# Optimization experiments

Measured on AMD Instinct MI355X. Metric: run time of the kernel, lower is better.

## Reference

```python
import jax, jax.numpy as jnp
import numpy as np

C = 512
GROUPS = 32
EPS = 1e-6

def setup_inputs() -> dict:
    key = jax.random.key(0)
    ks = jax.random.split(key, 6)
    s = 1.0 / np.sqrt(C)
    return {
        "x": jax.random.normal(ks[0], (2, C, 16, 32, 32), dtype=jnp.float32),
        "gamma": jnp.ones((C,), jnp.float32),
        "beta": jnp.zeros((C,), jnp.float32),
        "q_w": jax.random.normal(ks[1], (C, C), jnp.float32) * s,
        "q_b": jnp.zeros((C,), jnp.float32),
        "k_w": jax.random.normal(ks[2], (C, C), jnp.float32) * s,
        "k_b": jnp.zeros((C,), jnp.float32),
        "v_w": jax.random.normal(ks[3], (C, C), jnp.float32) * s,
        "v_b": jnp.zeros((C,), jnp.float32),
        "proj_w": jax.random.normal(ks[4], (C, C), jnp.float32) * s,
        "proj_b": jnp.zeros((C,), jnp.float32),
    }

def _group_norm(x, gamma, beta):
    # x: [b, c, t, h, w]
    b, c, t, h, w = x.shape
    xg = x.reshape(b, GROUPS, c // GROUPS, t, h, w)
    mean = xg.mean(axis=(2, 3, 4, 5), keepdims=True)
    var = xg.var(axis=(2, 3, 4, 5), keepdims=True)
    xg = (xg - mean) * jax.lax.rsqrt(var + EPS)
    x = xg.reshape(b, c, t, h, w)
    return x * gamma[None, :, None, None, None] + beta[None, :, None, None, None]

def _pw_conv(x, w, bias):
    # 1x1x1 conv == channel GEMM. x: [b,c,t,h,w], w: [c_out, c_in]
    y = jnp.einsum('bcthw,oc->bothw', x, w)
    return y + bias[None, :, None, None, None]

def reference(x, gamma, beta, q_w, q_b, k_w, k_b, v_w, v_b, proj_w, proj_b):
    b, c, t, h, w = x.shape
    hn = _group_norm(x, gamma, beta)
    q = _pw_conv(hn, q_w, q_b)
    k = _pw_conv(hn, k_w, k_b)
    v = _pw_conv(hn, v_w, v_b)
    # [b,c,t,h,w] -> [b*t, h*w, c]
    def to_seq(a):
        return jnp.transpose(a, (0, 2, 3, 4, 1)).reshape(b * t, h * w, c)
    q, k, v = to_seq(q), to_seq(k), to_seq(v)
    scale = 1.0 / jnp.sqrt(jnp.asarray(c, x.dtype))
    attn = jnp.einsum('bqc,bkc->bqk', q, k) * scale  # [b*t, hw, hw]
    attn = jax.nn.softmax(attn, axis=-1)
    out = jnp.einsum('bqk,bkc->bqc', attn, v)
    out = out.reshape(b, t, h, w, c).transpose(0, 4, 1, 2, 3)
    return x + _pw_conv(out, proj_w, proj_b)
```

## Files before the change

### kernel.cpp

```cpp
#include <hip/hip_runtime.h>

typedef unsigned short u16;
typedef __attribute__((ext_vector_type(8))) short bf16x8;
typedef __attribute__((ext_vector_type(4))) float f32x4;

#define DEV static __device__ __forceinline__

DEV u16 f2bf(float f) {
  union { float f; unsigned u; } x; x.f = f;
  return (u16)((x.u + 0x7FFFu + ((x.u >> 16) & 1u)) >> 16);
}
DEV float bf2f(u16 h) { union { unsigned u; float f; } x; x.u = ((unsigned)h) << 16; return x.f; }

DEV void gload16(const void* g, void* l) {
  __builtin_amdgcn_global_load_lds((const __attribute__((address_space(1))) void*)g,
                                   (__attribute__((address_space(3))) void*)l, 16, 0, 0);
}

__global__ __launch_bounds__(256) void gn_stats_a(const float* __restrict__ x,
                                                  float2* __restrict__ part) {
  const int bg = blockIdx.x >> 5, slice = blockIdx.x & 31;
  const float* base = x + (long)bg * 262144 + slice * 8192;
  float s = 0.f, q = 0.f;
#pragma unroll
  for (int i = 0; i < 8; ++i) {
    float4 v = *(const float4*)(base + i * 1024 + threadIdx.x * 4);
    s += v.x + v.y + v.z + v.w;
    q += v.x * v.x + v.y * v.y + v.z * v.z + v.w * v.w;
  }
#pragma unroll
  for (int o = 32; o; o >>= 1) { s += __shfl_xor(s, o); q += __shfl_xor(q, o); }
  __shared__ float2 red[4];
  if ((threadIdx.x & 63) == 0) red[threadIdx.x >> 6] = make_float2(s, q);
  __syncthreads();
  if (threadIdx.x == 0) {
    float S = 0.f, Q = 0.f;
    for (int i = 0; i < 4; ++i) { S += red[i].x; Q += red[i].y; }
    part[blockIdx.x] = make_float2(S, Q);
  }
}

__global__ void gn_stats_b(const float2* __restrict__ part, float2* __restrict__ stats) {
  float s = 0.f, q = 0.f;
  if (threadIdx.x < 32) {
    float2 p = part[blockIdx.x * 32 + threadIdx.x];
    s = p.x; q = p.y;
  }
#pragma unroll
  for (int o = 32; o; o >>= 1) { s += __shfl_xor(s, o); q += __shfl_xor(q, o); }
  if (threadIdx.x == 0) {
    const float inv = 1.f / 262144.f;
    float mean = s * inv;
    float var = q * inv - mean * mean;
    stats[blockIdx.x] = make_float2(mean, rsqrtf(var + 1e-6f));
  }
}

__global__ __launch_bounds__(256) void gn_apply(const float* __restrict__ x,
                                                const float* __restrict__ gamma,
                                                const float* __restrict__ beta,
                                                const float2* __restrict__ stats,
                                                u16* __restrict__ hn) {
  __shared__ u16 tile[64][65];
  const int p0 = blockIdx.x * 64, c0 = blockIdx.y * 64, bt = blockIdx.z;
  const int b = bt >> 4, t = bt & 15, tid = threadIdx.x;
  const float* xb = x + (long)b * 8388608 + t * 1024;
#pragma unroll 4
  for (int r = 0; r < 16; ++r) {
    int ci = r * 4 + (tid >> 6), pi = tid & 63;
    int c = c0 + ci;
    float2 st = stats[b * 32 + (c >> 4)];
    float v = xb[(long)c * 16384 + p0 + pi];
    v = (v - st.x) * st.y * gamma[c] + beta[c];
    tile[ci][pi] = f2bf(v);
  }
  __syncthreads();
  u16* hb = hn + ((long)bt * 1024 + p0) * 512 + c0;
#pragma unroll 4
  for (int r = 0; r < 16; ++r) {
    int pi = r * 4 + (tid >> 6), ci = tid & 63;
    hb[(long)pi * 512 + ci] = tile[ci][pi];
  }
}

__global__ __launch_bounds__(256) void wconv(const float* __restrict__ w0, const float* __restrict__ w1,
                                             const float* __restrict__ w2, const float* __restrict__ w3,
                                             u16* __restrict__ dst) {
  int e = (blockIdx.x * 256 + threadIdx.x) * 4;
  const float* src = w0;
  int which = e >> 18, off = e & 262143;
  if (which == 1) src = w1; else if (which == 2) src = w2; else if (which == 3) src = w3;
  float4 v = *(const float4*)(src + off);
  ushort4 o;
  o.x = f2bf(v.x); o.y = f2bf(v.y); o.z = f2bf(v.z); o.w = f2bf(v.w);
  *(ushort4*)(dst + e) = o;
}

__global__ void bcat(const float* __restrict__ qb, const float* __restrict__ kb,
                     const float* __restrict__ vb, float* __restrict__ dst) {
  int i = blockIdx.x * 256 + threadIdx.x;
  if (i < 512) dst[i] = qb[i];
  else if (i < 1024) dst[i] = kb[i - 512];
  else if (i < 1536) dst[i] = vb[i - 1024];
}

__global__ __launch_bounds__(256) void transpose_pc(const u16* __restrict__ v, int ldv,
                                                    u16* __restrict__ vT) {
  __shared__ u16 tile[64][65];
  const int p0 = blockIdx.x * 64, c0 = blockIdx.y * 64;
  const long bt = blockIdx.z;
  const int tid = threadIdx.x;
  const u16* vb = v + bt * 1024 * (long)ldv;
#pragma unroll 4
  for (int r = 0; r < 16; ++r) {
    int pi = r * 4 + (tid >> 6), ci = tid & 63;
    tile[pi][ci] = vb[(long)(p0 + pi) * ldv + c0 + ci];
  }
  __syncthreads();
  u16* ob = vT + bt * 524288;
#pragma unroll 4
  for (int r = 0; r < 16; ++r) {
    int ci = r * 4 + (tid >> 6), pi = tid & 63;
    ob[(long)(c0 + ci) * 1024 + p0 + pi] = tile[pi][ci];
  }
}

__global__ __launch_bounds__(256) void softmax_rows_bf16(u16* __restrict__ scores) {
  const int wave = threadIdx.x >> 6, lane = threadIdx.x & 63;
  const long row = (long)blockIdx.x * 4 + wave;
  u16* srow = scores + row * 1024;
  bf16x8 a0 = *(const bf16x8*)(srow + lane * 16);
  bf16x8 a1 = *(const bf16x8*)(srow + lane * 16 + 8);
  float v[16];
#pragma unroll
  for (int j = 0; j < 8; ++j) { v[j] = bf2f((u16)a0[j]); v[8 + j] = bf2f((u16)a1[j]); }
  float m = v[0];
#pragma unroll
  for (int j = 1; j < 16; ++j) m = fmaxf(m, v[j]);
#pragma unroll
  for (int o = 32; o; o >>= 1) m = fmaxf(m, __shfl_xor(m, o));
  const float sc = 0.044194173824159216f;
  float s = 0.f, e[16];
#pragma unroll
  for (int j = 0; j < 16; ++j) { e[j] = __expf((v[j] - m) * sc); s += e[j]; }
#pragma unroll
  for (int o = 32; o; o >>= 1) s += __shfl_xor(s, o);
  const float inv = 1.f / s;
  bf16x8 o0, o1;
#pragma unroll
  for (int j = 0; j < 8; ++j) {
    o0[j] = (short)f2bf(e[j] * inv);
    o1[j] = (short)f2bf(e[8 + j] * inv);
  }
  *(bf16x8*)(srow + lane * 16) = o0;
  *(bf16x8*)(srow + lane * 16 + 8) = o1;
}

template <bool OUT_BF16, bool HAS_BIAS>
__global__ __launch_bounds__(512, 2) void gemm256(
    const u16* __restrict__ A, int lda, long sA,
    const u16* __restrict__ B, int ldb, long sB,
    void* __restrict__ Cv, int ldc, long sC,
    const float* __restrict__ bias, int K) {
  __shared__ u16 sm[3 * 16384];
  const int tid = threadIdx.x;
  const int wid = tid >> 6, lane = tid & 63;
  const int wm = wid >> 2, wn = wid & 3;
  const long m0 = (long)blockIdx.x * 256;
  const long n0 = (long)blockIdx.y * 256;
  A += (long)blockIdx.z * sA + m0 * lda;
  B += (long)blockIdx.z * sB + n0 * ldb;
  const int NT = K >> 5;

  f32x4 acc[8][4] = {};

  const int r0 = tid >> 2;
  const int slot = (tid & 3) * 16;

  auto STAGE = [&](int kt, int b) {
    char* sA_ = (char*)&sm[b * 16384];
    char* sB_ = (char*)&sm[b * 16384 + 8192];
    const long kOff = (long)kt * 32;
#pragma unroll
    for (int i = 0; i < 2; ++i) {
      int row = i * 128 + r0;
      int cb = slot ^ (((row >> 1) & 3) << 4);
      gload16((const char*)(A + (long)row * lda + kOff) + cb, sA_ + i * 8192 + tid * 16);
      gload16((const char*)(B + (long)row * ldb + kOff) + cb, sB_ + i * 8192 + tid * 16);
    }
  };

  STAGE(0, 0);
  if (NT > 1) STAGE(1, 1);

  const int lrow = lane & 15;
  const int kslot = (lane >> 4) * 16;

  for (int t = 0; t < NT; ++t) {
    const int cur = t % 3;
    if (t + 2 < NT) {
      STAGE(t + 2, (t + 2) % 3);
      asm volatile("s_waitcnt vmcnt(8)" ::: "memory");
    } else if (t + 1 < NT) {
      asm volatile("s_waitcnt vmcnt(4)" ::: "memory");
    } else {
      asm volatile("s_waitcnt vmcnt(0)" ::: "memory");
    }
    __builtin_amdgcn_s_barrier();
    asm volatile("" ::: "memory");

    const char* bufA = (const char*)&sm[cur * 16384];
    const char* bufB = (const char*)&sm[cur * 16384 + 8192];
    bf16x8 af[8], bf[4];
#pragma unroll
    for (int mi = 0; mi < 8; ++mi) {
      int row = wm * 128 + mi * 16 + lrow;
      af[mi] = *(const bf16x8*)(bufA + row * 64 + (kslot ^ (((row >> 1) & 3) << 4)));
    }
#pragma unroll
    for (int ni = 0; ni < 4; ++ni) {
      int row = wn * 64 + ni * 16 + lrow;
      bf[ni] = *(const bf16x8*)(bufB + row * 64 + (kslot ^ (((row >> 1) & 3) << 4)));
    }
    __builtin_amdgcn_s_setprio(1);
#pragma unroll
    for (int mi = 0; mi < 8; ++mi)
#pragma unroll
      for (int ni = 0; ni < 4; ++ni)
        acc[mi][ni] = __builtin_amdgcn_mfma_f32_16x16x32_bf16(af[mi], bf[ni], acc[mi][ni], 0, 0, 0);
    __builtin_amdgcn_s_setprio(0);
    asm volatile("" ::: "memory");
    __builtin_amdgcn_s_barrier();
  }

  const int lc = lane & 15, lr = (lane >> 4) * 4;
  if (OUT_BF16) {
    u16* C = (u16*)Cv + (long)blockIdx.z * sC;
#pragma unroll
    for (int mi = 0; mi < 8; ++mi) {
      long r = m0 + wm * 128 + mi * 16 + lr;
#pragma unroll
      for (int ni = 0; ni < 4; ++ni) {
        long c = n0 + wn * 64 + ni * 16 + lc;
        float bv = HAS_BIAS ? bias[c] : 0.f;
#pragma unroll
        for (int j = 0; j < 4; ++j) C[(r + j) * ldc + c] = f2bf(acc[mi][ni][j] + bv);
      }
    }
  } else {
    float* C = (float*)Cv + (long)blockIdx.z * sC;
#pragma unroll
    for (int mi = 0; mi < 8; ++mi) {
      long r = m0 + wm * 128 + mi * 16 + lr;
#pragma unroll
      for (int ni = 0; ni < 4; ++ni) {
        long c = n0 + wn * 64 + ni * 16 + lc;
        float bv = HAS_BIAS ? bias[c] : 0.f;
#pragma unroll
        for (int j = 0; j < 4; ++j) C[(r + j) * ldc + c] = acc[mi][ni][j] + bv;
      }
    }
  }
}

__global__ __launch_bounds__(256) void final_write(const float* __restrict__ projout,
                                                   const float* __restrict__ proj_b,
                                                   const float* __restrict__ x,
                                                   float* __restrict__ out) {
  __shared__ float tile[64][65];
  const int p0 = blockIdx.x * 64, c0 = blockIdx.y * 64, bt = blockIdx.z;
  const int b = bt >> 4, t = bt & 15, tid = threadIdx.x;
  const float* pr = projout + ((long)bt * 1024 + p0) * 512 + c0;
#pragma unroll 4
  for (int r = 0; r < 16; ++r) {
    int pi = r * 4 + (tid >> 6), ci = tid & 63;
    tile[pi][ci] = pr[(long)pi * 512 + ci];
  }
  __syncthreads();
  const long obase = (long)b * 8388608 + t * 1024;
#pragma unroll 4
  for (int r = 0; r < 16; ++r) {
    int ci = r * 4 + (tid >> 6), pi = tid & 63;
    long idx = obase + (long)(c0 + ci) * 16384 + p0 + pi;
    out[idx] = x[idx] + proj_b[c0 + ci] + tile[pi][ci];
  }
}

extern "C" void kernel_launch(void* const* d_in, const int* in_sizes, int n_in,
                              void* d_out, int out_size, void* d_ws, size_t ws_size,
                              hipStream_t stream) {
  (void)in_sizes; (void)n_in; (void)out_size;
  const float* x      = (const float*)d_in[0];
  const float* gamma  = (const float*)d_in[1];
  const float* beta   = (const float*)d_in[2];
  const float* q_w    = (const float*)d_in[3];
  const float* q_b    = (const float*)d_in[4];
  const float* k_w    = (const float*)d_in[5];
  const float* k_b    = (const float*)d_in[6];
  const float* v_w    = (const float*)d_in[7];
  const float* v_b    = (const float*)d_in[8];
  const float* proj_w = (const float*)d_in[9];
  const float* proj_b = (const float*)d_in[10];

  const size_t OFF_WB    = 0;
  const size_t OFF_BIAS  = 2097152;
  const size_t OFF_STATS = 2103296;
  const size_t OFF_PART  = 2103808;
  const size_t OFF_HN    = 2121728;
  const size_t OFF_QKV   = 35676160;
  const size_t OFF_SC    = 136339456;

  char* ws = (char*)d_ws;
  u16*    wb      = (u16*)(ws + OFF_WB);
  float*  qkvbias = (float*)(ws + OFF_BIAS);
  float2* stats   = (float2*)(ws + OFF_STATS);
  float2* part    = (float2*)(ws + OFF_PART);
  u16*    hn      = (u16*)(ws + OFF_HN);
  u16*    vT      = hn;
  u16*    qkv     = (u16*)(ws + OFF_QKV);
  float*  projout = (float*)(ws + OFF_QKV);
  u16*    scores  = (u16*)(ws + OFF_SC);

  const int CH = (ws_size >= 237002752ULL) ? 32 : 8;
  u16* ob = (u16*)(ws + OFF_SC + (size_t)CH * 2097152);

  wconv<<<1024, 256, 0, stream>>>(q_w, k_w, v_w, proj_w, wb);
  bcat<<<6, 256, 0, stream>>>(q_b, k_b, v_b, qkvbias);
  gn_stats_a<<<2048, 256, 0, stream>>>(x, part);
  gn_stats_b<<<64, 64, 0, stream>>>(part, stats);
  gn_apply<<<dim3(16, 8, 32), 256, 0, stream>>>(x, gamma, beta, stats, hn);

  gemm256<true, true><<<dim3(128, 6, 1), 512, 0, stream>>>(
      hn, 512, 0, wb, 512, 0, qkv, 1536, 0, qkvbias, 512);

  transpose_pc<<<dim3(16, 8, 32), 256, 0, stream>>>(qkv + 1024, 1536, vT);

  for (int ch = 0; ch < 32 / CH; ++ch) {
    long f0 = (long)ch * CH;
    gemm256<true, false><<<dim3(4, 4, CH), 512, 0, stream>>>(
        qkv + f0 * 1572864, 1536, 1572864,
        qkv + 512 + f0 * 1572864, 1536, 1572864,
        scores, 1024, 1048576, nullptr, 512);
    softmax_rows_bf16<<<CH * 256, 256, 0, stream>>>(scores);
    gemm256<true, false><<<dim3(4, 2, CH), 512, 0, stream>>>(
        scores, 1024, 1048576,
        vT + f0 * 524288, 1024, 524288,
        ob + f0 * 524288, 512, 524288, nullptr, 1024);
  }

  gemm256<false, false><<<dim3(128, 2, 1), 512, 0, stream>>>(
      ob, 512, 0, wb + 786432, 512, 0, projout, 512, 0, nullptr, 512);
  final_write<<<dim3(16, 8, 32), 256, 0, stream>>>(projout, proj_b, x, (float*)d_out);
}
```

Measured before the change: 318.7 us.

## Restructure GEMM into 8-phase double-buffered pipeline with K=64 tiles and XCD remap

Replaces the triple-buffered K=32 GEMM mainloop with a double-buffered K=64 tile split into four sub-phases. Each phase issues a quarter of the next tile's global-to-LDS loads while running 16 MFMAs on the current tile. The LDS swizzle changes to a 128-byte row layout, and 2D grids are remapped so consecutive blocks go to the same XCD for better L2 locality. The extra barriers per iteration and the larger LDS footprint (128KB per block) may limit occupancy or add sync overhead.

```diff
diff --git a/kernel.cpp b/kernel.cpp
--- a/kernel.cpp
+++ b/kernel.cpp
@@ -156,81 +156,129 @@
   *(bf16x8*)(srow + lane * 16 + 8) = o1;
 }
 
+#define SYNC_MID() do { asm volatile("" ::: "memory"); __builtin_amdgcn_s_barrier(); \
+  asm volatile("s_waitcnt lgkmcnt(0)" ::: "memory"); __builtin_amdgcn_sched_barrier(0); } while (0)
+#define SYNC_END() do { asm volatile("" ::: "memory"); __builtin_amdgcn_s_barrier(); \
+  asm volatile("" ::: "memory"); } while (0)
+
 template <bool OUT_BF16, bool HAS_BIAS>
-__global__ __launch_bounds__(512, 2) void gemm256(
+__global__ __launch_bounds__(512, 2) void gemm8p(
     const u16* __restrict__ A, int lda, long sA,
     const u16* __restrict__ B, int ldb, long sB,
     void* __restrict__ Cv, int ldc, long sC,
     const float* __restrict__ bias, int K) {
-  __shared__ u16 sm[3 * 16384];
+  __shared__ u16 sm[2 * 32768];
   const int tid = threadIdx.x;
   const int wid = tid >> 6, lane = tid & 63;
   const int wm = wid >> 2, wn = wid & 3;
-  const long m0 = (long)blockIdx.x * 256;
-  const long n0 = (long)blockIdx.y * 256;
+
+  int bx = blockIdx.x, by = blockIdx.y;
+  if (gridDim.z == 1 && (((int)gridDim.x * (int)gridDim.y) & 7) == 0) {
+    int gy = gridDim.y;
+    int d = by * gridDim.x + bx;
+    int per = ((int)gridDim.x * gy) >> 3;
+    int w = (d & 7) * per + (d >> 3);
+    bx = w / gy; by = w % gy;
+  }
+  const long m0 = (long)bx * 256;
+  const long n0 = (long)by * 256;
   A += (long)blockIdx.z * sA + m0 * lda;
   B += (long)blockIdx.z * sB + n0 * ldb;
-  const int NT = K >> 5;
+  const int NT = K >> 6;
 
   f32x4 acc[8][4] = {};
 
-  const int r0 = tid >> 2;
-  const int slot = (tid & 3) * 16;
-
-  auto STAGE = [&](int kt, int b) {
-    char* sA_ = (char*)&sm[b * 16384];
-    char* sB_ = (char*)&sm[b * 16384 + 8192];
-    const long kOff = (long)kt * 32;
+  char* smc = (char*)sm;
+  auto STAGE_HALF = [&](int kt, int which) {
+    const char* src = (const char*)((which < 2) ? A : B);
+    const long ldby = 2L * ((which < 2) ? lda : ldb);
+    const int rowbase = (which & 1) * 128;
+    char* dst = smc + (kt & 1) * 65536 + ((which < 2) ? 0 : 32768) + rowbase * 128;
+    const char* gk = src + (long)kt * 128;
 #pragma unroll
     for (int i = 0; i < 2; ++i) {
-      int row = i * 128 + r0;
-      int cb = slot ^ (((row >> 1) & 3) << 4);
-      gload16((const char*)(A + (long)row * lda + kOff) + cb, sA_ + i * 8192 + tid * 16);
-      gload16((const char*)(B + (long)row * ldb + kOff) + cb, sB_ + i * 8192 + tid * 16);
+      int rl = i * 64 + (tid >> 3);
+      int cb = (tid & 7) * 16;
+      int scb = cb ^ ((rl & 7) << 4);
+      gload16(gk + (long)(rowbase + rl) * ldby + scb, dst + rl * 128 + cb);
     }
   };
 
-  STAGE(0, 0);
-  if (NT > 1) STAGE(1, 1);
-
-  const int lrow = lane & 15;
-  const int kslot = (lane >> 4) * 16;
-
-  for (int t = 0; t < NT; ++t) {
-    const int cur = t % 3;
-    if (t + 2 < NT) {
-      STAGE(t + 2, (t + 2) % 3);
-      asm volatile("s_waitcnt vmcnt(8)" ::: "memory");
-    } else if (t + 1 < NT) {
-      asm volatile("s_waitcnt vmcnt(4)" ::: "memory");
-    } else {
-      asm volatile("s_waitcnt vmcnt(0)" ::: "memory");
+  const int lrow = lane & 15, kslot = (lane >> 4) * 16;
+  auto RD_A = [&](int buf, int kk, int mh, bf16x8* af) {
+#pragma unroll
+    for (int mi = 0; mi < 4; ++mi) {
+      int row = wm * 128 + (mh * 4 + mi) * 16 + lrow;
+      int cb = (kk * 64 + kslot) ^ ((row & 7) << 4);
+      af[mi] = *(const bf16x8*)(smc + buf * 65536 + row * 128 + cb);
     }
-    __builtin_amdgcn_s_barrier();
-    asm volatile("" ::: "memory");
-
-    const char* bufA = (const char*)&sm[cur * 16384];
-    const char* bufB = (const char*)&sm[cur * 16384 + 8192];
-    bf16x8 af[8], bf[4];
-#pragma unroll
-    for (int mi = 0; mi < 8; ++mi) {
-      int row = wm * 128 + mi * 16 + lrow;
-      af[mi] = *(const bf16x8*)(bufA + row * 64 + (kslot ^ (((row >> 1) & 3) << 4)));
-    }
+  };
+  auto RD_B = [&](int buf, int kk, bf16x8* bf) {
 #pragma unroll
     for (int ni = 0; ni < 4; ++ni) {
       int row = wn * 64 + ni * 16 + lrow;
-      bf[ni] = *(const bf16x8*)(bufB + row * 64 + (kslot ^ (((row >> 1) & 3) << 4)));
+      int cb = (kk * 64 + kslot) ^ ((row & 7) << 4);
+      bf[ni] = *(const bf16x8*)(smc + buf * 65536 + 32768 + row * 128 + cb);
     }
+  };
+
+  STAGE_HALF(0, 0); STAGE_HALF(0, 1); STAGE_HALF(0, 2); STAGE_HALF(0, 3);
+  STAGE_HALF(1, 2);
+  asm volatile("s_waitcnt vmcnt(2)" ::: "memory");
+  SYNC_END();
+
+  for (int T = 0; T < NT; ++T) {
+    const int cur = T & 1;
+    const bool s1 = (T + 1 < NT), s2 = (T + 2 < NT);
+    bf16x8 af[4], bf[4];
+    RD_B(cur, 0, bf);
+    RD_A(cur, 0, 0, af);
+    if (s1) STAGE_HALF(T + 1, 0);
+    SYNC_MID();
     __builtin_amdgcn_s_setprio(1);
 #pragma unroll
-    for (int mi = 0; mi < 8; ++mi)
+    for (int mi = 0; mi < 4; ++mi)
 #pragma unroll
       for (int ni = 0; ni < 4; ++ni)
         acc[mi][ni] = __builtin_amdgcn_mfma_f32_16x16x32_bf16(af[mi], bf[ni], acc[mi][ni], 0, 0, 0);
     __builtin_amdgcn_s_setprio(0);
-    asm volatile("" ::: "memory");
-    __builtin_amdgcn_s_barrier();
+    SYNC_END();
+    RD_A(cur, 0, 1, af);
+    if (s1) STAGE_HALF(T + 1, 1);
+    SYNC_MID();
+    __builtin_amdgcn_s_setprio(1);
+#pragma unroll
+    for (int mi = 0; mi < 4; ++mi)
+#pragma unroll
+      for (int ni = 0; ni < 4; ++ni)
+        acc[4 + mi][ni] = __builtin_amdgcn_mfma_f32_16x16x32_bf16(af[mi], bf[ni], acc[4 + mi][ni], 0, 0, 0);
+    __builtin_amdgcn_s_setprio(0);
+    SYNC_END();
+    RD_B(cur, 1, bf);
+    RD_A(cur, 1, 0, af);
+    if (s1) STAGE_HALF(T + 1, 3);
+    SYNC_MID();
+    __builtin_amdgcn_s_setprio(1);
+#pragma unroll
+    for (int mi = 0; mi < 4; ++mi)
+#pragma unroll
+      for (int ni = 0; ni < 4; ++ni)
+        acc[mi][ni] = __builtin_amdgcn_mfma_f32_16x16x32_bf16(af[mi], bf[ni], acc[mi][ni], 0, 0, 0);
+    __builtin_amdgcn_s_setprio(0);
+    SYNC_END();
+    RD_A(cur, 1, 1, af);
+    if (s2) STAGE_HALF(T + 2, 2);
+    SYNC_MID();
+    __builtin_amdgcn_s_setprio(1);
+#pragma unroll
+    for (int mi = 0; mi < 4; ++mi)
+#pragma unroll
+      for (int ni = 0; ni < 4; ++ni)
+        acc[4 + mi][ni] = __builtin_amdgcn_mfma_f32_16x16x32_bf16(af[mi], bf[ni], acc[4 + mi][ni], 0, 0, 0);
+    __builtin_amdgcn_s_setprio(0);
+    if (s2) asm volatile("s_waitcnt vmcnt(2)" ::: "memory");
+    else    asm volatile("s_waitcnt vmcnt(0)" ::: "memory");
+    SYNC_END();
   }
 
   const int lc = lane & 15, lr = (lane >> 4) * 4;
@@ -330,25 +378,25 @@
   gn_stats_b<<<64, 64, 0, stream>>>(part, stats);
   gn_apply<<<dim3(16, 8, 32), 256, 0, stream>>>(x, gamma, beta, stats, hn);
 
-  gemm256<true, true><<<dim3(128, 6, 1), 512, 0, stream>>>(
+  gemm8p<true, true><<<dim3(128, 6, 1), 512, 0, stream>>>(
       hn, 512, 0, wb, 512, 0, qkv, 1536, 0, qkvbias, 512);
 
   transpose_pc<<<dim3(16, 8, 32), 256, 0, stream>>>(qkv + 1024, 1536, vT);
 
   for (int ch = 0; ch < 32 / CH; ++ch) {
     long f0 = (long)ch * CH;
-    gemm256<true, false><<<dim3(4, 4, CH), 512, 0, stream>>>(
+    gemm8p<true, false><<<dim3(4, 4, CH), 512, 0, stream>>>(
         qkv + f0 * 1572864, 1536, 1572864,
         qkv + 512 + f0 * 1572864, 1536, 1572864,
         scores, 1024, 1048576, nullptr, 512);
     softmax_rows_bf16<<<CH * 256, 256, 0, stream>>>(scores);
-    gemm256<true, false><<<dim3(4, 2, CH), 512, 0, stream>>>(
+    gemm8p<true, false><<<dim3(4, 2, CH), 512, 0, stream>>>(
         scores, 1024, 1048576,
         vT + f0 * 524288, 1024, 524288,
         ob + f0 * 524288, 512, 524288, nullptr, 1024);
   }
 
-  gemm256<false, false><<<dim3(128, 2, 1), 512, 0, stream>>>(
+  gemm8p<false, false><<<dim3(128, 2, 1), 512, 0, stream>>>(
       ob, 512, 0, wb + 786432, 512, 0, projout, 512, 0, nullptr, 512);
   final_write<<<dim3(16, 8, 32), 256, 0, stream>>>(projout, proj_b, x, (float*)d_out);
 }
```

Result: faster. 306.5 us (-3.8%).

## Fuse V transpose and residual output into GEMM epilogues with 128x256 tiles

Applied to the files above, without the earlier changes.

Replaces the 256x256 GEMM with a 128x256 tile kernel that allows higher occupancy, uses an XCD-aware block remap, and stages results through LDS for coalesced epilogue stores. The QKV GEMM now writes V directly transposed, and the projection GEMM adds bias and residual and writes the NCTHW output directly. This removes the separate transpose and final_write kernels and the fp32 projout round trip. The projection output is now rounded to bf16 before the residual add, which costs some precision.

```diff
diff --git a/kernel.cpp b/kernel.cpp
--- a/kernel.cpp
+++ b/kernel.cpp
@@ -104,27 +104,6 @@
   else if (i < 1536) dst[i] = vb[i - 1024];
 }
 
-__global__ __launch_bounds__(256) void transpose_pc(const u16* __restrict__ v, int ldv,
-                                                    u16* __restrict__ vT) {
-  __shared__ u16 tile[64][65];
-  const int p0 = blockIdx.x * 64, c0 = blockIdx.y * 64;
-  const long bt = blockIdx.z;
-  const int tid = threadIdx.x;
-  const u16* vb = v + bt * 1024 * (long)ldv;
-#pragma unroll 4
-  for (int r = 0; r < 16; ++r) {
-    int pi = r * 4 + (tid >> 6), ci = tid & 63;
-    tile[pi][ci] = vb[(long)(p0 + pi) * ldv + c0 + ci];
-  }
-  __syncthreads();
-  u16* ob = vT + bt * 524288;
-#pragma unroll 4
-  for (int r = 0; r < 16; ++r) {
-    int ci = r * 4 + (tid >> 6), pi = tid & 63;
-    ob[(long)(c0 + ci) * 1024 + p0 + pi] = tile[pi][ci];
-  }
-}
-
 __global__ __launch_bounds__(256) void softmax_rows_bf16(u16* __restrict__ scores) {
   const int wave = threadIdx.x >> 6, lane = threadIdx.x & 63;
   const long row = (long)blockIdx.x * 4 + wave;
@@ -156,133 +135,160 @@
   *(bf16x8*)(srow + lane * 16 + 8) = o1;
 }
 
-template <bool OUT_BF16, bool HAS_BIAS>
-__global__ __launch_bounds__(512, 2) void gemm256(
+template <int EPI>
+__global__ __launch_bounds__(512, 4) void gemmk(
     const u16* __restrict__ A, int lda, long sA,
     const u16* __restrict__ B, int ldb, long sB,
-    void* __restrict__ Cv, int ldc, long sC,
-    const float* __restrict__ bias, int K) {
-  __shared__ u16 sm[3 * 16384];
-  const int tid = threadIdx.x;
-  const int wid = tid >> 6, lane = tid & 63;
+    u16* __restrict__ Cv, int ldc, long sC,
+    const float* __restrict__ bias, int K,
+    const float* __restrict__ xin, float* __restrict__ outp,
+    u16* __restrict__ vT) {
+  __shared__ u16 sm[3 * 12288];
+  char* smc = (char*)sm;
+  const int tid = threadIdx.x, wid = tid >> 6, lane = tid & 63;
   const int wm = wid >> 2, wn = wid & 3;
-  const long m0 = (long)blockIdx.x * 256;
-  const long n0 = (long)blockIdx.y * 256;
-  A += (long)blockIdx.z * sA + m0 * lda;
-  B += (long)blockIdx.z * sB + n0 * ldb;
+
+  int bx = blockIdx.x, by = blockIdx.y, bz = blockIdx.z;
+  {
+    unsigned gx = gridDim.x, gy = gridDim.y;
+    unsigned total = gx * gy * gridDim.z;
+    if ((total & 7u) == 0) {
+      unsigned gxy = gx * gy;
+      unsigned d = (blockIdx.z * gy + blockIdx.y) * gx + blockIdx.x;
+      unsigned w = (d & 7u) * (total >> 3) + (d >> 3);
+      bz = w / gxy; unsigned r = w - (unsigned)bz * gxy;
+      bx = r / gy;  by = r - (unsigned)bx * gy;
+    }
+  }
+  const long m0 = (long)bx * 128, n0 = (long)by * 256;
+  const char* Ab = (const char*)(A + (long)bz * sA + m0 * lda);
+  const char* Bb = (const char*)(B + (long)bz * sB + n0 * ldb);
   const int NT = K >> 5;
-
-  f32x4 acc[8][4] = {};
-
-  const int r0 = tid >> 2;
-  const int slot = (tid & 3) * 16;
-
-  auto STAGE = [&](int kt, int b) {
-    char* sA_ = (char*)&sm[b * 16384];
-    char* sB_ = (char*)&sm[b * 16384 + 8192];
-    const long kOff = (long)kt * 32;
-#pragma unroll
-    for (int i = 0; i < 2; ++i) {
-      int row = i * 128 + r0;
-      int cb = slot ^ (((row >> 1) & 3) << 4);
-      gload16((const char*)(A + (long)row * lda + kOff) + cb, sA_ + i * 8192 + tid * 16);
-      gload16((const char*)(B + (long)row * ldb + kOff) + cb, sB_ + i * 8192 + tid * 16);
-    }
-  };
-
-  STAGE(0, 0);
-  if (NT > 1) STAGE(1, 1);
-
-  const int lrow = lane & 15;
-  const int kslot = (lane >> 4) * 16;
-
-  for (int t = 0; t < NT; ++t) {
-    const int cur = t % 3;
-    if (t + 2 < NT) {
-      STAGE(t + 2, (t + 2) % 3);
-      asm volatile("s_waitcnt vmcnt(8)" ::: "memory");
-    } else if (t + 1 < NT) {
-      asm volatile("s_waitcnt vmcnt(4)" ::: "memory");
-    } else {
-      asm volatile("s_waitcnt vmcnt(0)" ::: "memory");
-    }
-    __builtin_amdgcn_s_barrier();
-    asm volatile("" ::: "memory");
-
-    const char* bufA = (const char*)&sm[cur * 16384];
-    const char* bufB = (const char*)&sm[cur * 16384 + 8192];
-    bf16x8 af[8], bf[4];
-#pragma unroll
-    for (int mi = 0; mi < 8; ++mi) {
-      int row = wm * 128 + mi * 16 + lrow;
-      af[mi] = *(const bf16x8*)(bufA + row * 64 + (kslot ^ (((row >> 1) & 3) << 4)));
-    }
-#pragma unroll
-    for (int ni = 0; ni < 4; ++ni) {
-      int row = wn * 64 + ni * 16 + lrow;
-      bf[ni] = *(const bf16x8*)(bufB + row * 64 + (kslot ^ (((row >> 1) & 3) << 4)));
-    }
+  const long lda2 = 2L * lda, ldb2 = 2L * ldb;
+
+  const int srow = tid >> 2;
+  const int cb = ((tid & 3) * 16) ^ ((srow & 3) << 4);
+  const int dA = srow * 64 + (tid & 3) * 16;
+  const int dB0 = 8192 + dA, dB1 = 16384 + dA;
+  const char* gA  = Ab + (long)srow * lda2 + cb;
+  const char* gB0 = Bb + (long)srow * ldb2 + cb;
+  const char* gB1 = Bb + (long)(srow + 128) * ldb2 + cb;
+
+  const int lrow = lane & 15, kslot = (lane >> 4) * 16;
+  const int aoff = (wm * 64 + lrow) * 64 + (kslot ^ ((lrow & 3) << 4));
+  const int boff = 8192 + (wn * 64 + lrow) * 64 + (kslot ^ ((lrow & 3) << 4));
+
+  f32x4 acc[4][4] = {};
+
+#define STG3(off) do { gload16(gA, smc + (off) + dA); \
+                       gload16(gB0, smc + (off) + dB0); \
+                       gload16(gB1, smc + (off) + dB1); } while (0)
+
+  STG3(0);
+  gA += 64; gB0 += 64; gB1 += 64;
+  if (NT > 1) { STG3(24576); gA += 64; gB0 += 64; gB1 += 64; }
+  if (NT > 1) asm volatile("s_waitcnt vmcnt(3)" ::: "memory");
+  else        asm volatile("s_waitcnt vmcnt(0)" ::: "memory");
+  __builtin_amdgcn_s_barrier();
+
+  int cb_cur = 0, cb_stg = 49152;
+  for (int T = 0; T < NT; ++T) {
+    const bool s2 = (T + 2 < NT);
+    const char* ba = smc + cb_cur;
+    bf16x8 af[4], bf[4];
+#pragma unroll
+    for (int mi = 0; mi < 4; ++mi) af[mi] = *(const bf16x8*)(ba + aoff + mi * 1024);
+#pragma unroll
+    for (int ni = 0; ni < 4; ++ni) bf[ni] = *(const bf16x8*)(ba + boff + ni * 1024);
+    if (s2) { STG3(cb_stg); gA += 64; gB0 += 64; gB1 += 64; }
     __builtin_amdgcn_s_setprio(1);
 #pragma unroll
-    for (int mi = 0; mi < 8; ++mi)
+    for (int mi = 0; mi < 4; ++mi)
 #pragma unroll
       for (int ni = 0; ni < 4; ++ni)
         acc[mi][ni] = __builtin_amdgcn_mfma_f32_16x16x32_bf16(af[mi], bf[ni], acc[mi][ni], 0, 0, 0);
     __builtin_amdgcn_s_setprio(0);
-    asm volatile("" ::: "memory");
+    if (s2) asm volatile("s_waitcnt vmcnt(3)" ::: "memory");
+    else    asm volatile("s_waitcnt vmcnt(0)" ::: "memory");
     __builtin_amdgcn_s_barrier();
-  }
-
-  const int lc = lane & 15, lr = (lane >> 4) * 4;
-  if (OUT_BF16) {
-    u16* C = (u16*)Cv + (long)blockIdx.z * sC;
-#pragma unroll
-    for (int mi = 0; mi < 8; ++mi) {
-      long r = m0 + wm * 128 + mi * 16 + lr;
-#pragma unroll
-      for (int ni = 0; ni < 4; ++ni) {
-        long c = n0 + wn * 64 + ni * 16 + lc;
-        float bv = HAS_BIAS ? bias[c] : 0.f;
-#pragma unroll
-        for (int j = 0; j < 4; ++j) C[(r + j) * ldc + c] = f2bf(acc[mi][ni][j] + bv);
+    cb_cur = (cb_cur == 49152) ? 0 : cb_cur + 24576;
+    cb_stg = (cb_stg == 49152) ? 0 : cb_stg + 24576;
+  }
+#undef STG3
+
+  __syncthreads();
+  {
+    const int lc = lane & 15, lr = (lane >> 4) * 4;
+    char* wb_ = smc + wid * 8192;
+#pragma unroll
+    for (int ni = 0; ni < 4; ++ni) {
+      float bv = 0.f;
+      if (EPI == 1) bv = bias[n0 + wn * 64 + ni * 16 + lc];
+#pragma unroll
+      for (int mi = 0; mi < 4; ++mi)
+#pragma unroll
+        for (int j = 0; j < 4; ++j) {
+          int rml = mi * 16 + lr + j;
+          int colb = (ni * 32 + lc * 2) ^ ((rml & 7) << 4);
+          *(u16*)(wb_ + rml * 128 + colb) = f2bf(acc[mi][ni][j] + bv);
+        }
+    }
+  }
+  __syncthreads();
+
+  if (EPI == 2) {
+    const int bt = (int)(m0 >> 10), p0i = (int)(m0 & 1023);
+    const int b = bt >> 4, t = bt & 15;
+    const int c = tid & 255, pg = tid >> 8;
+    const long base = (long)b * 8388608 + (n0 + c) * 16384L + t * 1024 + p0i + pg * 64;
+    const float bv = bias[n0 + c];
+    const char* rb = smc + ((pg << 2) | (c >> 6)) * 8192;
+    const int c2 = (c & 63) * 2;
+#pragma unroll
+    for (int i = 0; i < 8; ++i) {
+      float vals[8];
+#pragma unroll
+      for (int j = 0; j < 8; ++j) {
+        int rl = i * 8 + j;
+        vals[j] = bf2f(*(const u16*)(rb + rl * 128 + (c2 ^ ((rl & 7) << 4))));
       }
+      float4 x0 = *(const float4*)(xin + base + i * 8);
+      float4 x1 = *(const float4*)(xin + base + i * 8 + 4);
+      float4 o0 = make_float4(x0.x + bv + vals[0], x0.y + bv + vals[1],
+                              x0.z + bv + vals[2], x0.w + bv + vals[3]);
+      float4 o1 = make_float4(x1.x + bv + vals[4], x1.y + bv + vals[5],
+                              x1.z + bv + vals[6], x1.w + bv + vals[7]);
+      *(float4*)(outp + base + i * 8) = o0;
+      *(float4*)(outp + base + i * 8 + 4) = o1;
+    }
+  } else if (EPI == 1 && n0 >= 1024) {
+    const int bt = (int)(m0 >> 10), p0i = (int)(m0 & 1023);
+    const int c = tid & 255, pg = tid >> 8;
+    u16* dst = vT + (long)bt * 524288 + (n0 - 1024 + c) * 1024 + p0i + pg * 64;
+    const char* rb = smc + ((pg << 2) | (c >> 6)) * 8192;
+    const int c2 = (c & 63) * 2;
+#pragma unroll
+    for (int i = 0; i < 8; ++i) {
+      u16 tmp[8];
+#pragma unroll
+      for (int j = 0; j < 8; ++j) {
+        int rl = i * 8 + j;
+        tmp[j] = *(const u16*)(rb + rl * 128 + (c2 ^ ((rl & 7) << 4)));
+      }
+      *(bf16x8*)(dst + i * 8) = *(bf16x8*)tmp;
     }
   } else {
-    float* C = (float*)Cv + (long)blockIdx.z * sC;
-#pragma unroll
-    for (int mi = 0; mi < 8; ++mi) {
-      long r = m0 + wm * 128 + mi * 16 + lr;
-#pragma unroll
-      for (int ni = 0; ni < 4; ++ni) {
-        long c = n0 + wn * 64 + ni * 16 + lc;
-        float bv = HAS_BIAS ? bias[c] : 0.f;
-#pragma unroll
-        for (int j = 0; j < 4; ++j) C[(r + j) * ldc + c] = acc[mi][ni][j] + bv;
-      }
-    }
-  }
-}
-
-__global__ __launch_bounds__(256) void final_write(const float* __restrict__ projout,
-                                                   const float* __restrict__ proj_b,
-                                                   const float* __restrict__ x,
-                                                   float* __restrict__ out) {
-  __shared__ float tile[64][65];
-  const int p0 = blockIdx.x * 64, c0 = blockIdx.y * 64, bt = blockIdx.z;
-  const int b = bt >> 4, t = bt & 15, tid = threadIdx.x;
-  const float* pr = projout + ((long)bt * 1024 + p0) * 512 + c0;
-#pragma unroll 4
-  for (int r = 0; r < 16; ++r) {
-    int pi = r * 4 + (tid >> 6), ci = tid & 63;
-    tile[pi][ci] = pr[(long)pi * 512 + ci];
-  }
-  __syncthreads();
-  const long obase = (long)b * 8388608 + t * 1024;
-#pragma unroll 4
-  for (int r = 0; r < 16; ++r) {
-    int ci = r * 4 + (tid >> 6), pi = tid & 63;
-    long idx = obase + (long)(c0 + ci) * 16384 + p0 + pi;
-    out[idx] = x[idx] + proj_b[c0 + ci] + tile[pi][ci];
+    u16* C = Cv + (long)bz * sC;
+    const int c8 = tid & 31, r0e = tid >> 5;
+#pragma unroll
+    for (int i = 0; i < 8; ++i) {
+      int r = r0e + i * 16;
+      int rwid = ((r >> 6) << 2) | (c8 >> 3);
+      int rr = r & 63;
+      bf16x8 v = *(const bf16x8*)(smc + rwid * 8192 + rr * 128 +
+                                  (((c8 & 7) * 16) ^ ((rr & 7) << 4)));
+      *(bf16x8*)(C + (m0 + r) * (long)ldc + n0 + c8 * 8) = v;
+    }
   }
 }
 
@@ -307,7 +313,8 @@
   const size_t OFF_STATS = 2103296;
   const size_t OFF_PART  = 2103808;
   const size_t OFF_HN    = 2121728;
-  const size_t OFF_QKV   = 35676160;
+  const size_t OFF_QK    = 35676160;
+  const size_t OFF_VT    = 102785024;
   const size_t OFF_SC    = 136339456;
 
   char* ws = (char*)d_ws;
@@ -316,13 +323,12 @@
   float2* stats   = (float2*)(ws + OFF_STATS);
   float2* part    = (float2*)(ws + OFF_PART);
   u16*    hn      = (u16*)(ws + OFF_HN);
-  u16*    vT      = hn;
-  u16*    qkv     = (u16*)(ws + OFF_QKV);
-  float*  projout = (float*)(ws + OFF_QKV);
+  u16*    ob      = hn;
+  u16*    qk      = (u16*)(ws + OFF_QK);
+  u16*    vT      = (u16*)(ws + OFF_VT);
   u16*    scores  = (u16*)(ws + OFF_SC);
 
-  const int CH = (ws_size >= 237002752ULL) ? 32 : 8;
-  u16* ob = (u16*)(ws + OFF_SC + (size_t)CH * 2097152);
+  const int CH = (ws_size >= OFF_SC + 32ULL * 2097152) ? 32 : 8;
 
   wconv<<<1024, 256, 0, stream>>>(q_w, k_w, v_w, proj_w, wb);
   bcat<<<6, 256, 0, stream>>>(q_b, k_b, v_b, qkvbias);
@@ -330,25 +336,23 @@
   gn_stats_b<<<64, 64, 0, stream>>>(part, stats);
   gn_apply<<<dim3(16, 8, 32), 256, 0, stream>>>(x, gamma, beta, stats, hn);
 
-  gemm256<true, true><<<dim3(128, 6, 1), 512, 0, stream>>>(
-      hn, 512, 0, wb, 512, 0, qkv, 1536, 0, qkvbias, 512);
-
-  transpose_pc<<<dim3(16, 8, 32), 256, 0, stream>>>(qkv + 1024, 1536, vT);
+  gemmk<1><<<dim3(256, 6, 1), 512, 0, stream>>>(
+      hn, 512, 0, wb, 512, 0, qk, 1024, 0, qkvbias, 512, nullptr, nullptr, vT);
 
   for (int ch = 0; ch < 32 / CH; ++ch) {
     long f0 = (long)ch * CH;
-    gemm256<true, false><<<dim3(4, 4, CH), 512, 0, stream>>>(
-        qkv + f0 * 1572864, 1536, 1572864,
-        qkv + 512 + f0 * 1572864, 1536, 1572864,
-        scores, 1024, 1048576, nullptr, 512);
+    gemmk<0><<<dim3(8, 4, CH), 512, 0, stream>>>(
+        qk + f0 * 1048576, 1024, 1048576,
+        qk + 512 + f0 * 1048576, 1024, 1048576,
+        scores, 1024, 1048576, nullptr, 512, nullptr, nullptr, nullptr);
     softmax_rows_bf16<<<CH * 256, 256, 0, stream>>>(scores);
-    gemm256<true, false><<<dim3(4, 2, CH), 512, 0, stream>>>(
+    gemmk<0><<<dim3(8, 2, CH), 512, 0, stream>>>(
         scores, 1024, 1048576,
         vT + f0 * 524288, 1024, 524288,
-        ob + f0 * 524288, 512, 524288, nullptr, 1024);
-  }
-
-  gemm256<false, false><<<dim3(128, 2, 1), 512, 0, stream>>>(
-      ob, 512, 0, wb + 786432, 512, 0, projout, 512, 0, nullptr, 512);
-  final_write<<<dim3(16, 8, 32), 256, 0, stream>>>(projout, proj_b, x, (float*)d_out);
-}
+        ob + f0 * 524288, 512, 524288, nullptr, 1024, nullptr, nullptr, nullptr);
+  }
+
+  gemmk<2><<<dim3(256, 2, 1), 512, 0, stream>>>(
+      ob, 512, 0, wb + 786432, 512, 0, nullptr, 0, 0, proj_b, 512,
+      x, (float*)d_out, nullptr);
+}
```

Result: faster. 288.1 us (-9.6%).
